# Kernel tuning notes

Hardware: AMD Instinct MI355X
Metric: run time of the kernel (lower is better)

The kernel has to match this reference:

```python
import jax, jax.numpy as jnp
import numpy as np

B, C, H, W = 4, 64, 160, 160
OUT, KH, KW = 64, 3, 3
STRIDE, PAD = 1, 1
K2 = KH * KW


def conv2d(x, w, b=None, stride=STRIDE, pad=PAD):
    y = jax.lax.conv_general_dilated(
        x, w, window_strides=(stride, stride),
        padding=[(pad, pad), (pad, pad)],
        dimension_numbers=("NCHW", "OIHW", "NCHW"))
    if b is not None:
        y = y + b[None, :, None, None]
    return y


def bilinear_gather(x, py, px):
    # x: [B,C,H,W]; py,px: [B,K2,Ho,Wo] float sampling positions
    Bq, Cq, Hq, Wq = x.shape
    y0 = jnp.floor(py)
    x0 = jnp.floor(px)
    wy1 = py - y0  # frac
    wx1 = px - x0
    y0i = y0.astype(jnp.int32)
    x0i = x0.astype(jnp.int32)
    x_flat = x.reshape(Bq, Cq, Hq * Wq)

    def corner(yi, xi, wgt):
        valid = (yi >= 0) & (yi < Hq) & (xi >= 0) & (xi < Wq)
        idx = jnp.clip(yi, 0, Hq - 1) * Wq + jnp.clip(xi, 0, Wq - 1)  # [B,K2,Ho,Wo]
        g = jax.vmap(lambda xf, i: jnp.take(xf, i, axis=1))(x_flat, idx)  # [B,C,K2,Ho,Wo]
        return g * (wgt * valid)[:, None]

    out = corner(y0i, x0i, (1 - wy1) * (1 - wx1))
    out = out + corner(y0i, x0i + 1, (1 - wy1) * wx1)
    out = out + corner(y0i + 1, x0i, wy1 * (1 - wx1))
    out = out + corner(y0i + 1, x0i + 1, wy1 * wx1)
    return out  # [B,C,K2,Ho,Wo]


def deform_forward(x, offset_w, offset_b, mask_w, mask_b, dcn_w):
    offset = conv2d(x, offset_w, offset_b)                # [B, 2*K2, Ho, Wo]
    mask = jax.nn.sigmoid(conv2d(x, mask_w, mask_b))      # [B, K2, Ho, Wo]
    Bq, _, Ho, Wo = offset.shape
    off = offset.reshape(Bq, K2, 2, Ho, Wo)
    off_y, off_x = off[:, :, 0], off[:, :, 1]
    k = jnp.arange(K2)
    ky = (k // KW).astype(jnp.float32)
    kx = (k % KW).astype(jnp.float32)
    base_i = jnp.arange(Ho, dtype=jnp.float32) * STRIDE - PAD
    base_j = jnp.arange(Wo, dtype=jnp.float32) * STRIDE - PAD
    py = off_y + base_i[None, None, :, None] + ky[None, :, None, None]
    px = off_x + base_j[None, None, None, :] + kx[None, :, None, None]
    sampled = bilinear_gather(x, py, px)                  # [B,C,K2,Ho,Wo]
    w = dcn_w.reshape(OUT, C, K2)
    # out[b,o,i,j] = sum_{c,k} w[o,c,k] * mask[b,k,i,j] * sampled[b,c,k,i,j]
    return jnp.einsum("ock,bckij,bkij->boij", w, sampled, mask)


def setup_inputs() -> dict:
    key = jax.random.key(0)
    ks = jax.random.split(key, 6)
    x = jax.random.normal(ks[0], (B, C, H, W), dtype=jnp.float32)
    # small random weights so offsets stay modest (module inits them to 0;
    # random values exercise the full deformable math)
    offset_w = jax.random.normal(ks[1], (2 * K2, C, KH, KW), dtype=jnp.float32) * 0.01
    offset_b = jax.random.normal(ks[2], (2 * K2,), dtype=jnp.float32) * 0.1
    mask_w = jax.random.normal(ks[3], (K2, C, KH, KW), dtype=jnp.float32) * 0.01
    mask_b = jax.random.normal(ks[4], (K2,), dtype=jnp.float32) * 0.1
    dcn_w = jax.random.normal(ks[5], (OUT, C, KH, KW), dtype=jnp.float32) * (1.0 / np.sqrt(C * K2))
    return {"x": x, "offset_w": offset_w, "offset_b": offset_b,
            "mask_w": mask_w, "mask_b": mask_b, "dcn_w": dcn_w}


def reference(x, offset_w, offset_b, mask_w, mask_b, dcn_w):
    return deform_forward(x, offset_w, offset_b, mask_w, mask_b, dcn_w)
```

## Files before the change

### kernel.cpp

```cpp
#include <hip/hip_runtime.h>
#include <math.h>

#define Bq 4
#define Cq 64
#define Hq 160
#define Wq 160
#define HWq (Hq*Wq)
#define OUTq 64
#define KKq 576
#define KS  18
#define SROW 584
#define HSTRIDE 72

typedef __attribute__((ext_vector_type(8))) _Float16 half8;
typedef __attribute__((ext_vector_type(2))) _Float16 half2v;
typedef __attribute__((ext_vector_type(4))) float float4v;
typedef unsigned short ushort_t;
typedef unsigned int uint_t;

__device__ __forceinline__ ushort_t f2h(float f) {
    return __builtin_bit_cast(ushort_t, (_Float16)f);
}
__device__ __forceinline__ uint_t f2hdup(float f) {
    uint_t u = (uint_t)f2h(f);
    return u | (u << 16);
}
__device__ __forceinline__ half2v h2(uint_t u) {
    return __builtin_bit_cast(half2v, u);
}
#define MFMA16(a,b,c) __builtin_amdgcn_mfma_f32_16x16x32_f16((a),(b),(c),0,0,0)

__global__ void __launch_bounds__(256) k_prep(const float* __restrict__ x,
                                              const float* __restrict__ dcn_w,
                                              const float* __restrict__ off_w,
                                              const float* __restrict__ msk_w,
                                              ushort_t* __restrict__ xt,
                                              ushort_t* __restrict__ wtf,
                                              ushort_t* __restrict__ cwf2) {
    __shared__ float tile[64][65];
    int b = blockIdx.y, hw0 = blockIdx.x * 64;
    int tid = threadIdx.x;
    int l16 = tid & 15, crow = tid >> 4;
#pragma unroll
    for (int i = 0; i < 4; ++i) {
        int c = crow + i*16;
        float4 v = *(const float4*)(x + ((size_t)(b*Cq + c))*HWq + hw0 + l16*4);
        tile[c][l16*4+0] = v.x;
        tile[c][l16*4+1] = v.y;
        tile[c][l16*4+2] = v.z;
        tile[c][l16*4+3] = v.w;
    }
    __syncthreads();
#pragma unroll
    for (int it = 0; it < 4; ++it) {
        int hw = (tid >> 4) + it*16;
        int c4 = (tid & 15) * 4;
        uint_t v0 = (uint_t)f2h(tile[c4+0][hw]) | ((uint_t)f2h(tile[c4+1][hw]) << 16);
        uint_t v1 = (uint_t)f2h(tile[c4+2][hw]) | ((uint_t)f2h(tile[c4+3][hw]) << 16);
        uint2 vv; vv.x = v0; vv.y = v1;
        *(uint2*)(xt + ((size_t)b*HWq + hw0 + hw)*64 + c4) = vv;
    }
    if (blockIdx.y == 0 && blockIdx.x < 216) {
        int id = blockIdx.x*256 + tid;
        if (id < 4*KS*512) {
            int j = id & 7, ln = (id>>3) & 63, ks = (id>>9) % KS, g = id/(512*KS);
            int kk = ks*32 + (ln>>4)*8 + j;
            int c  = kk & 63, kt = kk >> 6;
            int m  = g*16 + (ln&15);
            wtf[id] = f2h(dcn_w[m*KKq + c*9 + kt]);
        }
        int id2 = id - 4*KS*512;
        if (id2 >= 0 && id2 < 9*2*2*512) {
            int j = id2 & 7, ln = (id2>>3) & 63;
            int ks2 = (id2>>9) & 1, g = (id2>>10) & 1, k = id2 >> 11;
            int co = g*16 + (ln&15);
            int c  = ks2*32 + (ln>>4)*8 + j;
            float w = 0.f;
            if (co < 18)      w = off_w[co*KKq + c*9 + k];
            else if (co < 27) w = msk_w[(co-18)*KKq + c*9 + k];
            cwf2[id2] = f2h(w);
        }
    }
}

__global__ void __launch_bounds__(256, 6) k_fused(const ushort_t* __restrict__ xt,
                                                  const ushort_t* __restrict__ cwf2,
                                                  const float* __restrict__ off_b,
                                                  const float* __restrict__ msk_b,
                                                  const ushort_t* __restrict__ wtf,
                                                  float* __restrict__ out) {
    __shared__ __align__(16) char s_mem[16*SROW*2];
    __shared__ __align__(16) uint4 s_A[144];
    __shared__ __align__(16) uint4 s_W[144];
    ushort_t* halo   = (ushort_t*)s_mem;
    float*    s_part = (float*)(s_mem + 7776);
    ushort_t* s_s    = (ushort_t*)s_mem;

    int bid = blockIdx.x;
    int blk = (bid & 7) * 800 + (bid >> 3);
    int jt = blk % 10, i = (blk/10) % Hq, b = blk/(10*Hq);
    int j0 = jt*16;
    int tid = threadIdx.x, lane = tid & 63, grp = tid >> 6;
    int n = lane & 15, quad = lane >> 4;

    int gM = grp & 1, kh = grp >> 1;
    half8 af[9];
#pragma unroll
    for (int s = 0; s < 9; ++s) {
        int st = kh*9 + s;
        int k = st >> 1, ks2 = st & 1;
        af[s] = *(const half8*)(cwf2 + (size_t)(((k*2+gM)*2+ks2)*512 + lane*8));
    }

    const ushort_t* xtb = xt + (size_t)b*HWq*64;
#pragma unroll
    for (int t = tid; t < 432; t += 256) {
        int seg = t >> 3, sub = t & 7;
        int ky = seg / 18, px = seg % 18;
        int y = i + ky - 1, xx = j0 + px - 1;
        uint4 v = {0u,0u,0u,0u};
        if (y >= 0 && y < Hq && xx >= 0 && xx < Wq)
            v = *(const uint4*)(xtb + ((size_t)y*Wq + xx)*64 + sub*8);
        *(uint4*)(halo + (ky*18 + px)*HSTRIDE + sub*8) = v;
    }
    __syncthreads();

    {
        float4v cacc = {0.f,0.f,0.f,0.f};
#pragma unroll
        for (int s = 0; s < 9; ++s) {
            int st = kh*9 + s;
            int k = st >> 1, ks2 = st & 1;
            int ky = k/3, kx = k - (k/3)*3;
            half8 bf = *(const half8*)(halo + (ky*18 + n + kx)*HSTRIDE + quad*8 + ks2*32);
            cacc = MFMA16(af[s], bf, cacc);
        }
        *(float4v*)(s_part + grp*256 + lane*4) = cacc;
    }
    __syncthreads();

    if (tid < 144) {
        int p = tid & 15, k = tid >> 4;
        #define RD(co) (s_part[(((co)>>4)*256)     + ((((co)&15)>>2)*16 + p)*4 + ((co)&3)] + \
                        s_part[(2 + ((co)>>4))*256 + ((((co)&15)>>2)*16 + p)*4 + ((co)&3)])
        float oy = RD(2*k)   + off_b[2*k];
        float ox = RD(2*k+1) + off_b[2*k+1];
        float mv = RD(18+k)  + msk_b[k];
        #undef RD
        float m = 1.f/(1.f + __expf(-mv));
        float py = oy + (float)(i - 1 + k/3);
        float px = ox + (float)(j0 + p - 1 + (k - (k/3)*3));
        float fy = floorf(py), fx = floorf(px);
        int y0 = (int)fy, x0 = (int)fx;
        float wy1 = py - fy, wx1 = px - fx;
        float wy0 = 1.f - wy1, wx0 = 1.f - wx1;
        bool vy0 = (y0 >= 0) & (y0 < Hq),   vy1 = (y0+1 >= 0) & (y0+1 < Hq);
        bool vx0 = (x0 >= 0) & (x0 < Wq),   vx1 = (x0+1 >= 0) & (x0+1 < Wq);
        int yc0 = min(max(y0,   0), Hq-1), yc1 = min(max(y0+1, 0), Hq-1);
        int xc0 = min(max(x0,   0), Wq-1), xc1 = min(max(x0+1, 0), Wq-1);
        s_A[tid] = make_uint4((uint_t)((yc0*Wq + xc0)*128),
                              (uint_t)((yc0*Wq + xc1)*128),
                              (uint_t)((yc1*Wq + xc0)*128),
                              (uint_t)((yc1*Wq + xc1)*128));
        s_W[tid] = make_uint4(f2hdup((vy0 && vx0) ? wy0*wx0*m : 0.f),
                              f2hdup((vy0 && vx1) ? wy0*wx1*m : 0.f),
                              f2hdup((vy1 && vx0) ? wy1*wx0*m : 0.f),
                              f2hdup((vy1 && vx1) ? wy1*wx1*m : 0.f));
    }
    __syncthreads();

    {
        int lane4 = (lane & 31) * 4;
        int halfi = lane >> 5;
        const char* xtbB = (const char*)xtb;
        char* s_sb = (char*)s_s;
        int tb = grp*2 + halfi;
        uint4 Wd[3];
        uint_t u[3][4];
#pragma unroll
        for (int q = 0; q < 3; ++q) {
            uint4 A = s_A[tb + q*8];
            Wd[q]   = s_W[tb + q*8];
            u[q][0] = *(const uint_t*)(xtbB + A.x + lane4);
            u[q][1] = *(const uint_t*)(xtbB + A.y + lane4);
            u[q][2] = *(const uint_t*)(xtbB + A.z + lane4);
            u[q][3] = *(const uint_t*)(xtbB + A.w + lane4);
        }
#pragma unroll
        for (int iter = 0; iter < 18; ++iter) {
            const int q = iter % 3;
            uint4 Wc = Wd[q];
            uint_t v0 = u[q][0], v1 = u[q][1], v2 = u[q][2], v3 = u[q][3];
            if (iter + 3 < 18) {
                uint4 A = s_A[tb + (iter+3)*8];
                Wd[q]   = s_W[tb + (iter+3)*8];
                u[q][0] = *(const uint_t*)(xtbB + A.x + lane4);
                u[q][1] = *(const uint_t*)(xtbB + A.y + lane4);
                u[q][2] = *(const uint_t*)(xtbB + A.z + lane4);
                u[q][3] = *(const uint_t*)(xtbB + A.w + lane4);
            }
            uint_t dst = (uint_t)(tb*(SROW*2) + (iter & 1)*(8*SROW*2) + (iter >> 1)*128);
            half2v acc2 = h2(v0) * h2(Wc.x);
            acc2 = __builtin_elementwise_fma(h2(v1), h2(Wc.y), acc2);
            acc2 = __builtin_elementwise_fma(h2(v2), h2(Wc.z), acc2);
            acc2 = __builtin_elementwise_fma(h2(v3), h2(Wc.w), acc2);
            *(uint_t*)(s_sb + dst + lane4) = __builtin_bit_cast(uint_t, acc2);
        }
    }
    __syncthreads();

    float4v acc = {0.f,0.f,0.f,0.f};
    const ushort_t* arow = wtf + ((size_t)(grp*KS)*64 + lane)*8;
    const ushort_t* brow = s_s + n*SROW + quad*8;
    half8 a_cur = *(const half8*)(arow);
#pragma unroll
    for (int ks = 0; ks < KS; ++ks) {
        half8 a_next = a_cur;
        if (ks < KS-1) a_next = *(const half8*)(arow + (ks+1)*512);
        half8 bf = *(const half8*)(brow + ks*32);
        acc = MFMA16(a_cur, bf, acc);
        a_cur = a_next;
    }

#pragma unroll
    for (int r = 0; r < 4; ++r) {
        int o = grp*16 + quad*4 + r;
        out[(((size_t)b*OUTq + o)*Hq + i)*Wq + j0 + n] = acc[r];
    }
}

extern "C" void kernel_launch(void* const* d_in, const int* in_sizes, int n_in,
                              void* d_out, int out_size, void* d_ws, size_t ws_size,
                              hipStream_t stream) {
    const float* x     = (const float*)d_in[0];
    const float* off_w = (const float*)d_in[1];
    const float* off_b = (const float*)d_in[2];
    const float* msk_w = (const float*)d_in[3];
    const float* msk_b = (const float*)d_in[4];
    const float* dcn_w = (const float*)d_in[5];
    float* out = (float*)d_out;

    char* ws = (char*)d_ws;
    ushort_t* xt   = (ushort_t*)ws;
    ushort_t* wtf  = xt + (size_t)Bq*HWq*64;
    ushort_t* cwf2 = wtf + 4*KS*512;

    hipLaunchKernelGGL(k_prep, dim3(HWq/64, Bq), dim3(256), 0, stream,
                       x, dcn_w, off_w, msk_w, xt, wtf, cwf2);
    hipLaunchKernelGGL(k_fused, dim3(Bq*Hq*10), dim3(256), 0, stream,
                       xt, cwf2, off_b, msk_b, wtf, out);
}
```

Baseline: 131.0 us.

## Drop LDS halo staging and widen bilinear gather to 8-byte loads

```diff
diff --git a/kernel.cpp b/kernel.cpp
--- a/kernel.cpp
+++ b/kernel.cpp
@@ -10,7 +10,6 @@
 #define KKq 576
 #define KS  18
 #define SROW 584
-#define HSTRIDE 72
 
 typedef __attribute__((ext_vector_type(8))) _Float16 half8;
 typedef __attribute__((ext_vector_type(2))) _Float16 half2v;
@@ -92,8 +91,7 @@
     __shared__ __align__(16) char s_mem[16*SROW*2];
     __shared__ __align__(16) uint4 s_A[144];
     __shared__ __align__(16) uint4 s_W[144];
-    ushort_t* halo   = (ushort_t*)s_mem;
-    float*    s_part = (float*)(s_mem + 7776);
+    float*    s_part = (float*)s_mem;
     ushort_t* s_s    = (ushort_t*)s_mem;
 
     int bid = blockIdx.x;
@@ -113,17 +111,6 @@
     }
 
     const ushort_t* xtb = xt + (size_t)b*HWq*64;
-#pragma unroll
-    for (int t = tid; t < 432; t += 256) {
-        int seg = t >> 3, sub = t & 7;
-        int ky = seg / 18, px = seg % 18;
-        int y = i + ky - 1, xx = j0 + px - 1;
-        uint4 v = {0u,0u,0u,0u};
-        if (y >= 0 && y < Hq && xx >= 0 && xx < Wq)
-            v = *(const uint4*)(xtb + ((size_t)y*Wq + xx)*64 + sub*8);
-        *(uint4*)(halo + (ky*18 + px)*HSTRIDE + sub*8) = v;
-    }
-    __syncthreads();
 
     {
         float4v cacc = {0.f,0.f,0.f,0.f};
@@ -132,8 +119,14 @@
             int st = kh*9 + s;
             int k = st >> 1, ks2 = st & 1;
             int ky = k/3, kx = k - (k/3)*3;
-            half8 bf = *(const half8*)(halo + (ky*18 + n + kx)*HSTRIDE + quad*8 + ks2*32);
-            cacc = MFMA16(af[s], bf, cacc);
+            int y  = i + ky - 1;
+            int xx = j0 + n + kx - 1;
+            int yc = min(max(y, 0), Hq-1);
+            int xc = min(max(xx, 0), Wq-1);
+            uint4 raw = *(const uint4*)(xtb + ((size_t)yc*Wq + xc)*64 + quad*8 + ks2*32);
+            uint_t msk = ((y >= 0) & (y < Hq) & (xx >= 0) & (xx < Wq)) ? 0xFFFFFFFFu : 0u;
+            raw.x &= msk; raw.y &= msk; raw.z &= msk; raw.w &= msk;
+            cacc = MFMA16(af[s], __builtin_bit_cast(half8, raw), cacc);
         }
         *(float4v*)(s_part + grp*256 + lane*4) = cacc;
     }
@@ -170,41 +163,42 @@
     __syncthreads();
 
     {
-        int lane4 = (lane & 31) * 4;
-        int halfi = lane >> 5;
+        int sub = lane >> 4;
+        int ch8 = (lane & 15) * 8;
+        int q16 = grp*4 + sub;
         const char* xtbB = (const char*)xtb;
         char* s_sb = (char*)s_s;
-        int tb = grp*2 + halfi;
-        uint4 Wd[3];
-        uint_t u[3][4];
-#pragma unroll
-        for (int q = 0; q < 3; ++q) {
-            uint4 A = s_A[tb + q*8];
-            Wd[q]   = s_W[tb + q*8];
-            u[q][0] = *(const uint_t*)(xtbB + A.x + lane4);
-            u[q][1] = *(const uint_t*)(xtbB + A.y + lane4);
-            u[q][2] = *(const uint_t*)(xtbB + A.z + lane4);
-            u[q][3] = *(const uint_t*)(xtbB + A.w + lane4);
-        }
-#pragma unroll
-        for (int iter = 0; iter < 18; ++iter) {
-            const int q = iter % 3;
-            uint4 Wc = Wd[q];
-            uint_t v0 = u[q][0], v1 = u[q][1], v2 = u[q][2], v3 = u[q][3];
-            if (iter + 3 < 18) {
-                uint4 A = s_A[tb + (iter+3)*8];
-                Wd[q]   = s_W[tb + (iter+3)*8];
-                u[q][0] = *(const uint_t*)(xtbB + A.x + lane4);
-                u[q][1] = *(const uint_t*)(xtbB + A.y + lane4);
-                u[q][2] = *(const uint_t*)(xtbB + A.z + lane4);
-                u[q][3] = *(const uint_t*)(xtbB + A.w + lane4);
+        uint_t dstb = (uint_t)(q16*(SROW*2) + ch8);
+        uint4 A  = s_A[q16];
+        uint4 Wt = s_W[q16];
+        uint2 u00 = *(const uint2*)(xtbB + A.x + ch8);
+        uint2 u01 = *(const uint2*)(xtbB + A.y + ch8);
+        uint2 u10 = *(const uint2*)(xtbB + A.z + ch8);
+        uint2 u11 = *(const uint2*)(xtbB + A.w + ch8);
+#pragma unroll
+        for (int iter = 0; iter < 9; ++iter) {
+            uint4 Wc = Wt;
+            uint2 v00 = u00, v01 = u01, v10 = u10, v11 = u11;
+            if (iter < 8) {
+                A  = s_A[(iter+1)*16 + q16];
+                Wt = s_W[(iter+1)*16 + q16];
+                u00 = *(const uint2*)(xtbB + A.x + ch8);
+                u01 = *(const uint2*)(xtbB + A.y + ch8);
+                u10 = *(const uint2*)(xtbB + A.z + ch8);
+                u11 = *(const uint2*)(xtbB + A.w + ch8);
             }
-            uint_t dst = (uint_t)(tb*(SROW*2) + (iter & 1)*(8*SROW*2) + (iter >> 1)*128);
-            half2v acc2 = h2(v0) * h2(Wc.x);
-            acc2 = __builtin_elementwise_fma(h2(v1), h2(Wc.y), acc2);
-            acc2 = __builtin_elementwise_fma(h2(v2), h2(Wc.z), acc2);
-            acc2 = __builtin_elementwise_fma(h2(v3), h2(Wc.w), acc2);
-            *(uint_t*)(s_sb + dst + lane4) = __builtin_bit_cast(uint_t, acc2);
+            half2v lo = h2(v00.x) * h2(Wc.x);
+            half2v hi = h2(v00.y) * h2(Wc.x);
+            lo = __builtin_elementwise_fma(h2(v01.x), h2(Wc.y), lo);
+            hi = __builtin_elementwise_fma(h2(v01.y), h2(Wc.y), hi);
+            lo = __builtin_elementwise_fma(h2(v10.x), h2(Wc.z), lo);
+            hi = __builtin_elementwise_fma(h2(v10.y), h2(Wc.z), hi);
+            lo = __builtin_elementwise_fma(h2(v11.x), h2(Wc.w), lo);
+            hi = __builtin_elementwise_fma(h2(v11.y), h2(Wc.w), hi);
+            uint2 res;
+            res.x = __builtin_bit_cast(uint_t, lo);
+            res.y = __builtin_bit_cast(uint_t, hi);
+            *(uint2*)(s_sb + dstb + iter*128) = res;
         }
     }
     __syncthreads();
```

Result: slower. 159.8 us (+22.0%).
